# Performance work log

Hardware: AMD Instinct MI355X
Metric: run time of the kernel (lower is better)

Reference implementation:

```python
import jax, jax.numpy as jnp
import numpy as np

B, N, D = 256, 196, 768  # batch, num_patches (14x14 grid), patch_dim (16*16*3)


def setup_inputs() -> dict:
    key = jax.random.key(0)
    k1, k2 = jax.random.split(key)
    features = jax.random.normal(k1, (B, N, D), dtype=jnp.float32)
    position_logits = jax.random.normal(k2, (B, N, N), dtype=jnp.float32)
    return {"features": features, "position_logits": position_logits}


def _rearrange_patches(patches, pos):
    # Deterministic gather form: for each target slot p, take the LARGEST j with
    # pos[i, j] == p, else leave the zero-init.
    b, n, d = patches.shape
    j_ids = jnp.arange(n, dtype=jnp.int32)
    match = pos[:, :, None] == jnp.arange(n)[None, None, :]          # [B, j, p]
    winner = jnp.max(jnp.where(match, j_ids[None, :, None], -1), axis=1)  # [B, p]
    gathered = jnp.take_along_axis(patches, jnp.clip(winner, 0)[:, :, None], axis=1)
    return jnp.where(winner[:, :, None] >= 0, gathered, jnp.zeros((), patches.dtype))


def reference(features, position_logits):
    b, n, d = features.shape
    g = int(n ** 0.5)
    # _get_position_predictions: argmax / max-softmax over dim=1 (position classes)
    pos = jnp.argmax(position_logits, axis=1)                         # [B, N] int
    confidence = jnp.max(jax.nn.softmax(position_logits, axis=1), axis=1)  # [B, N]
    # _rearrange_patches (scatter by predicted position)
    patches = _rearrange_patches(features, pos)
    # _smooth_edges: 3-tap average over interior patch indices, reading originals
    mid = (patches[:, :-2] + patches[:, 1:-1] + patches[:, 2:]) / 3.0
    patches = jnp.concatenate([patches[:, :1], mid, patches[:, -1:]], axis=1)
    # _reconstruct_image: [B, g, g, D] -> [B, D, g, g]
    img = patches.reshape(b, g, g, d).transpose(0, 3, 1, 2)
    return img, confidence
```

## Files before the change

kernel.cpp:

```cpp
#include <hip/hip_runtime.h>
#include <math.h>

#define BB 256
#define NN 196
#define DD 768
#define TDK 32
#define PSTRIDE 204
#define NW 16

typedef float f32x4 __attribute__((ext_vector_type(4)));

__global__ __launch_bounds__(1024) void pos_conf_kernel(
    const float* __restrict__ logits,
    float* __restrict__ conf_out,
    int* __restrict__ winner_out)
{
    const int b = blockIdx.x;
    const int t = threadIdx.x;
    const int w = t >> 6;
    const int l = t & 63;

    __shared__ float sm[NW][NN];
    __shared__ float ss[NW][NN];
    __shared__ int   si[NW][NN];
    __shared__ int   winner_s[NN];

    if (t < NN) winner_s[t] = -1;

    const int i0 = (49 * w) >> 2;
    const int i1 = (49 * (w + 1)) >> 2;

    if (l < 49) {
        const float* base = logits + (size_t)b * NN * NN + 4 * l;
        f32x4 m = {-INFINITY, -INFINITY, -INFINITY, -INFINITY};
        f32x4 s = {0.f, 0.f, 0.f, 0.f};
        int4 idx = make_int4(0, 0, 0, 0);
        #pragma unroll 4
        for (int i = i0; i < i1; ++i) {
            const f32x4 x = *reinterpret_cast<const f32x4*>(base + (size_t)i * NN);
            f32x4 mn;
            mn.x = fmaxf(m.x, x.x); mn.y = fmaxf(m.y, x.y);
            mn.z = fmaxf(m.z, x.z); mn.w = fmaxf(m.w, x.w);
            idx.x = (x.x > m.x) ? i : idx.x;
            idx.y = (x.y > m.y) ? i : idx.y;
            idx.z = (x.z > m.z) ? i : idx.z;
            idx.w = (x.w > m.w) ? i : idx.w;
            s.x = s.x * __expf(m.x - mn.x) + __expf(x.x - mn.x);
            s.y = s.y * __expf(m.y - mn.y) + __expf(x.y - mn.y);
            s.z = s.z * __expf(m.z - mn.z) + __expf(x.z - mn.z);
            s.w = s.w * __expf(m.w - mn.w) + __expf(x.w - mn.w);
            m = mn;
        }
        const int c = 4 * l;
        sm[w][c + 0] = m.x; ss[w][c + 0] = s.x; si[w][c + 0] = idx.x;
        sm[w][c + 1] = m.y; ss[w][c + 1] = s.y; si[w][c + 1] = idx.y;
        sm[w][c + 2] = m.z; ss[w][c + 2] = s.z; si[w][c + 2] = idx.z;
        sm[w][c + 3] = m.w; ss[w][c + 3] = s.w; si[w][c + 3] = idx.w;
    }
    __syncthreads();

    if (t < NN) {
        const int j = t;
        float m = -INFINITY;
        int idx = 0;
        #pragma unroll
        for (int ww = 0; ww < NW; ++ww) {
            const float mg = sm[ww][j];
            if (mg > m) { m = mg; idx = si[ww][j]; }
        }
        float s = 0.0f;
        #pragma unroll
        for (int ww = 0; ww < NW; ++ww)
            s += ss[ww][j] * __expf(sm[ww][j] - m);
        conf_out[b * NN + j] = 1.0f / s;
        atomicMax(&winner_s[idx], j);
    }
    __syncthreads();
    if (t < NN) winner_out[b * NN + t] = winner_s[t];
}

__global__ __launch_bounds__(256) void rearrange_kernel(
    const float* __restrict__ features,
    const int* __restrict__ winner,
    float* __restrict__ img)
{
    const int b  = blockIdx.y;
    const int d0 = blockIdx.x * TDK;
    const int t  = threadIdx.x;

    __shared__ float tile[TDK][PSTRIDE];

    const float* fb = features + (size_t)b * NN * DD;
    const int* wb = winner + b * NN;

    int w[7];
    #pragma unroll
    for (int i = 0; i < 7; ++i) {
        const int r = (t >> 3) + 32 * i;
        w[i] = (r < NN) ? wb[r] : -1;
    }

    const int d4 = (t & 7) * 4;
    #pragma unroll
    for (int i = 0; i < 7; ++i) {
        const int r = (t >> 3) + 32 * i;
        if (r < NN) {
            float4 v = make_float4(0.f, 0.f, 0.f, 0.f);
            if (w[i] >= 0)
                v = *reinterpret_cast<const float4*>(fb + (size_t)w[i] * DD + d0 + d4);
            tile[d4 + 0][r] = v.x;
            tile[d4 + 1][r] = v.y;
            tile[d4 + 2][r] = v.z;
            tile[d4 + 3][r] = v.w;
        }
    }
    __syncthreads();

    #pragma unroll
    for (int it = 0; it < 7; ++it) {
        const int q = t + 256 * it;
        if (q < TDK * 49) {
            const int d = q / 49;
            const int c = q - 49 * d;
            const int p0 = 4 * c;
            const float4 ctr = *reinterpret_cast<const float4*>(&tile[d][p0]);
            const float left  = tile[d][p0 > 0 ? p0 - 1 : 0];
            const float right = tile[d][p0 + 4 < NN ? p0 + 4 : NN - 1];
            f32x4 o;
            o.x = (p0 == 0)          ? ctr.x : (left  + ctr.x + ctr.y) * (1.0f / 3.0f);
            o.y = (ctr.x + ctr.y + ctr.z) * (1.0f / 3.0f);
            o.z = (ctr.y + ctr.z + ctr.w) * (1.0f / 3.0f);
            o.w = (p0 + 3 == NN - 1) ? ctr.w : (ctr.z + ctr.w + right) * (1.0f / 3.0f);
            float* dst = img + (size_t)b * DD * NN + (size_t)(d0 + d) * NN + p0;
            __builtin_nontemporal_store(o, reinterpret_cast<f32x4*>(dst));
        }
    }
}

extern "C" void kernel_launch(void* const* d_in, const int* in_sizes, int n_in,
                              void* d_out, int out_size, void* d_ws, size_t ws_size,
                              hipStream_t stream) {
    const float* features = (const float*)d_in[0];
    const float* logits   = (const float*)d_in[1];

    float* out  = (float*)d_out;
    float* img  = out;
    float* conf = out + (size_t)BB * DD * NN;
    int*   winner = (int*)d_ws;

    pos_conf_kernel<<<BB, 1024, 0, stream>>>(logits, conf, winner);

    dim3 grid(DD / TDK, BB);
    rearrange_kernel<<<grid, 256, 0, stream>>>(features, winner, img);
}
```

Before: 53.65 us.

## Fuse position argmax and rearrange/smooth into one per-batch kernel

After: 50.53 us. 1.06x faster.

```diff
diff --git a/kernel.cpp b/kernel.cpp
--- a/kernel.cpp
+++ b/kernel.cpp
@@ -5,57 +5,62 @@
 #define NN 196
 #define DD 768
 #define TDK 32
+#define NTILES (DD / TDK)
 #define PSTRIDE 204
 #define NW 16
 
 typedef float f32x4 __attribute__((ext_vector_type(4)));
 
-__global__ __launch_bounds__(1024) void pos_conf_kernel(
+__global__ __launch_bounds__(1024) void fused_kernel(
+    const float* __restrict__ features,
     const float* __restrict__ logits,
-    float* __restrict__ conf_out,
-    int* __restrict__ winner_out)
+    float* __restrict__ img,
+    float* __restrict__ conf_out)
 {
     const int b = blockIdx.x;
     const int t = threadIdx.x;
-    const int w = t >> 6;
-    const int l = t & 63;
 
     __shared__ float sm[NW][NN];
     __shared__ float ss[NW][NN];
     __shared__ int   si[NW][NN];
     __shared__ int   winner_s[NN];
+    __shared__ float tile[TDK][PSTRIDE];
+
+    const int wv = t >> 6;
+    const int l  = t & 63;
 
     if (t < NN) winner_s[t] = -1;
 
-    const int i0 = (49 * w) >> 2;
-    const int i1 = (49 * (w + 1)) >> 2;
-
-    if (l < 49) {
-        const float* base = logits + (size_t)b * NN * NN + 4 * l;
-        f32x4 m = {-INFINITY, -INFINITY, -INFINITY, -INFINITY};
-        f32x4 s = {0.f, 0.f, 0.f, 0.f};
-        int4 idx = make_int4(0, 0, 0, 0);
-        #pragma unroll 4
-        for (int i = i0; i < i1; ++i) {
-            const f32x4 x = *reinterpret_cast<const f32x4*>(base + (size_t)i * NN);
-            f32x4 mn;
-            mn.x = fmaxf(m.x, x.x); mn.y = fmaxf(m.y, x.y);
-            mn.z = fmaxf(m.z, x.z); mn.w = fmaxf(m.w, x.w);
-            idx.x = (x.x > m.x) ? i : idx.x;
-            idx.y = (x.y > m.y) ? i : idx.y;
-            idx.z = (x.z > m.z) ? i : idx.z;
-            idx.w = (x.w > m.w) ? i : idx.w;
-            s.x = s.x * __expf(m.x - mn.x) + __expf(x.x - mn.x);
-            s.y = s.y * __expf(m.y - mn.y) + __expf(x.y - mn.y);
-            s.z = s.z * __expf(m.z - mn.z) + __expf(x.z - mn.z);
-            s.w = s.w * __expf(m.w - mn.w) + __expf(x.w - mn.w);
-            m = mn;
+    {
+        const int i0 = (49 * wv) >> 2;
+        const int i1 = (49 * (wv + 1)) >> 2;
+        if (l < 49) {
+            const float* basep = logits + (size_t)b * NN * NN + 4 * l;
+            f32x4 m = {-INFINITY, -INFINITY, -INFINITY, -INFINITY};
+            f32x4 s = {0.f, 0.f, 0.f, 0.f};
+            int4 idx = make_int4(0, 0, 0, 0);
+            #pragma unroll 4
+            for (int i = i0; i < i1; ++i) {
+                const f32x4 x = *reinterpret_cast<const f32x4*>(basep + (size_t)i * NN);
+                f32x4 mn;
+                mn.x = fmaxf(m.x, x.x); mn.y = fmaxf(m.y, x.y);
+                mn.z = fmaxf(m.z, x.z); mn.w = fmaxf(m.w, x.w);
+                idx.x = (x.x > m.x) ? i : idx.x;
+                idx.y = (x.y > m.y) ? i : idx.y;
+                idx.z = (x.z > m.z) ? i : idx.z;
+                idx.w = (x.w > m.w) ? i : idx.w;
+                s.x = s.x * __expf(m.x - mn.x) + __expf(x.x - mn.x);
+                s.y = s.y * __expf(m.y - mn.y) + __expf(x.y - mn.y);
+                s.z = s.z * __expf(m.z - mn.z) + __expf(x.z - mn.z);
+                s.w = s.w * __expf(m.w - mn.w) + __expf(x.w - mn.w);
+                m = mn;
+            }
+            const int c = 4 * l;
+            sm[wv][c + 0] = m.x; ss[wv][c + 0] = s.x; si[wv][c + 0] = idx.x;
+            sm[wv][c + 1] = m.y; ss[wv][c + 1] = s.y; si[wv][c + 1] = idx.y;
+            sm[wv][c + 2] = m.z; ss[wv][c + 2] = s.z; si[wv][c + 2] = idx.z;
+            sm[wv][c + 3] = m.w; ss[wv][c + 3] = s.w; si[wv][c + 3] = idx.w;
         }
-        const int c = 4 * l;
-        sm[w][c + 0] = m.x; ss[w][c + 0] = s.x; si[w][c + 0] = idx.x;
-        sm[w][c + 1] = m.y; ss[w][c + 1] = s.y; si[w][c + 1] = idx.y;
-        sm[w][c + 2] = m.z; ss[w][c + 2] = s.z; si[w][c + 2] = idx.z;
-        sm[w][c + 3] = m.w; ss[w][c + 3] = s.w; si[w][c + 3] = idx.w;
     }
     __syncthreads();
 
@@ -76,64 +81,67 @@
         atomicMax(&winner_s[idx], j);
     }
     __syncthreads();
-    if (t < NN) winner_out[b * NN + t] = winner_s[t];
-}
-
-__global__ __launch_bounds__(256) void rearrange_kernel(
-    const float* __restrict__ features,
-    const int* __restrict__ winner,
-    float* __restrict__ img)
-{
-    const int b  = blockIdx.y;
-    const int d0 = blockIdx.x * TDK;
-    const int t  = threadIdx.x;
-
-    __shared__ float tile[TDK][PSTRIDE];
 
     const float* fb = features + (size_t)b * NN * DD;
-    const int* wb = winner + b * NN;
+    float* ob = img + (size_t)b * DD * NN;
 
-    int w[7];
-    #pragma unroll
-    for (int i = 0; i < 7; ++i) {
-        const int r = (t >> 3) + 32 * i;
-        w[i] = (r < NN) ? wb[r] : -1;
-    }
+    const int q1_ok = (t < 1568 - 1024);
+    const int r0 = t >> 3;
+    const int d40 = (t & 7) * 4;
+    const int r1 = (t + 1024) >> 3;
+    const int d41 = ((t + 1024) & 7) * 4;
 
-    const int d4 = (t & 7) * 4;
-    #pragma unroll
-    for (int i = 0; i < 7; ++i) {
-        const int r = (t >> 3) + 32 * i;
-        if (r < NN) {
-            float4 v = make_float4(0.f, 0.f, 0.f, 0.f);
-            if (w[i] >= 0)
-                v = *reinterpret_cast<const float4*>(fb + (size_t)w[i] * DD + d0 + d4);
-            tile[d4 + 0][r] = v.x;
-            tile[d4 + 1][r] = v.y;
-            tile[d4 + 2][r] = v.z;
-            tile[d4 + 3][r] = v.w;
+    const int w0 = winner_s[r0];
+    const int w1 = q1_ok ? winner_s[r1] : -1;
+
+    const f32x4 zero = {0.f, 0.f, 0.f, 0.f};
+    f32x4 v0 = zero, v1 = zero, nv0 = zero, nv1 = zero;
+
+    if (w0 >= 0) v0 = *reinterpret_cast<const f32x4*>(fb + (size_t)w0 * DD + d40);
+    if (w1 >= 0) v1 = *reinterpret_cast<const f32x4*>(fb + (size_t)w1 * DD + d41);
+
+    for (int k = 0; k < NTILES; ++k) {
+        tile[d40 + 0][r0] = v0.x;
+        tile[d40 + 1][r0] = v0.y;
+        tile[d40 + 2][r0] = v0.z;
+        tile[d40 + 3][r0] = v0.w;
+        if (q1_ok) {
+            tile[d41 + 0][r1] = v1.x;
+            tile[d41 + 1][r1] = v1.y;
+            tile[d41 + 2][r1] = v1.z;
+            tile[d41 + 3][r1] = v1.w;
         }
-    }
-    __syncthreads();
 
-    #pragma unroll
-    for (int it = 0; it < 7; ++it) {
-        const int q = t + 256 * it;
-        if (q < TDK * 49) {
-            const int d = q / 49;
-            const int c = q - 49 * d;
-            const int p0 = 4 * c;
-            const float4 ctr = *reinterpret_cast<const float4*>(&tile[d][p0]);
-            const float left  = tile[d][p0 > 0 ? p0 - 1 : 0];
-            const float right = tile[d][p0 + 4 < NN ? p0 + 4 : NN - 1];
-            f32x4 o;
-            o.x = (p0 == 0)          ? ctr.x : (left  + ctr.x + ctr.y) * (1.0f / 3.0f);
-            o.y = (ctr.x + ctr.y + ctr.z) * (1.0f / 3.0f);
-            o.z = (ctr.y + ctr.z + ctr.w) * (1.0f / 3.0f);
-            o.w = (p0 + 3 == NN - 1) ? ctr.w : (ctr.z + ctr.w + right) * (1.0f / 3.0f);
-            float* dst = img + (size_t)b * DD * NN + (size_t)(d0 + d) * NN + p0;
-            __builtin_nontemporal_store(o, reinterpret_cast<f32x4*>(dst));
+        if (k + 1 < NTILES) {
+            const int d0n = (k + 1) * TDK;
+            nv0 = zero; nv1 = zero;
+            if (w0 >= 0) nv0 = *reinterpret_cast<const f32x4*>(fb + (size_t)w0 * DD + d0n + d40);
+            if (w1 >= 0) nv1 = *reinterpret_cast<const f32x4*>(fb + (size_t)w1 * DD + d0n + d41);
         }
+        __syncthreads();
+
+        const int d0 = k * TDK;
+        #pragma unroll
+        for (int it = 0; it < 2; ++it) {
+            const int q = t + 1024 * it;
+            if (q < TDK * 49) {
+                const int d = q / 49;
+                const int c = q - 49 * d;
+                const int p0 = 4 * c;
+                const f32x4 ctr = *reinterpret_cast<const f32x4*>(&tile[d][p0]);
+                const float left  = tile[d][p0 > 0 ? p0 - 1 : 0];
+                const float right = tile[d][p0 + 4 < NN ? p0 + 4 : NN - 1];
+                f32x4 o;
+                o.x = (p0 == 0)          ? ctr.x : (left  + ctr.x + ctr.y) * (1.0f / 3.0f);
+                o.y = (ctr.x + ctr.y + ctr.z) * (1.0f / 3.0f);
+                o.z = (ctr.y + ctr.z + ctr.w) * (1.0f / 3.0f);
+                o.w = (p0 + 3 == NN - 1) ? ctr.w : (ctr.z + ctr.w + right) * (1.0f / 3.0f);
+                float* dst = ob + (size_t)(d0 + d) * NN + p0;
+                __builtin_nontemporal_store(o, reinterpret_cast<f32x4*>(dst));
+            }
+        }
+        v0 = nv0; v1 = nv1;
+        __syncthreads();
     }
 }
 
@@ -146,10 +154,6 @@
     float* out  = (float*)d_out;
     float* img  = out;
     float* conf = out + (size_t)BB * DD * NN;
-    int*   winner = (int*)d_ws;
 
-    pos_conf_kernel<<<BB, 1024, 0, stream>>>(logits, conf, winner);
-
-    dim3 grid(DD / TDK, BB);
-    rearrange_kernel<<<grid, 256, 0, stream>>>(features, winner, img);
+    fused_kernel<<<BB, 1024, 0, stream>>>(features, logits, img, conf);
 }
```

## Split position kernel across column halves with global atomic winners and swizzled LDS tile

Applied to the files above, without the earlier changes.

Measured after the change: 56.17 us. 1.05x slower.

```diff
diff --git a/kernel.cpp b/kernel.cpp
--- a/kernel.cpp
+++ b/kernel.cpp
@@ -5,134 +5,132 @@
 #define NN 196
 #define DD 768
 #define TDK 32
-#define PSTRIDE 204
-#define NW 16
+#define NTILES (DD / TDK)
+#define SROW 224
+#define NITEMS (NN * 8)
 
 typedef float f32x4 __attribute__((ext_vector_type(4)));
+typedef float f32x2 __attribute__((ext_vector_type(2)));
 
-__global__ __launch_bounds__(1024) void pos_conf_kernel(
+__global__ __launch_bounds__(512) void pos_conf_kernel(
     const float* __restrict__ logits,
     float* __restrict__ conf_out,
-    int* __restrict__ winner_out)
+    int* __restrict__ winner_g)
 {
     const int b = blockIdx.x;
+    const int h = blockIdx.y;
     const int t = threadIdx.x;
-    const int w = t >> 6;
-    const int l = t & 63;
+    const int wv = t >> 6;
+    const int l  = t & 63;
 
-    __shared__ float sm[NW][NN];
-    __shared__ float ss[NW][NN];
-    __shared__ int   si[NW][NN];
-    __shared__ int   winner_s[NN];
+    __shared__ float sm[8][98];
+    __shared__ float ss[8][98];
+    __shared__ int   si[8][98];
 
-    if (t < NN) winner_s[t] = -1;
-
-    const int i0 = (49 * w) >> 2;
-    const int i1 = (49 * (w + 1)) >> 2;
+    const int i0 = (49 * wv) >> 1;
+    const int i1 = (49 * (wv + 1)) >> 1;
 
     if (l < 49) {
-        const float* base = logits + (size_t)b * NN * NN + 4 * l;
-        f32x4 m = {-INFINITY, -INFINITY, -INFINITY, -INFINITY};
-        f32x4 s = {0.f, 0.f, 0.f, 0.f};
-        int4 idx = make_int4(0, 0, 0, 0);
+        const float* basep = logits + (size_t)b * NN * NN + 98 * h + 2 * l;
+        f32x2 m = {-INFINITY, -INFINITY};
+        f32x2 s = {0.f, 0.f};
+        int2 idx = make_int2(0, 0);
         #pragma unroll 4
         for (int i = i0; i < i1; ++i) {
-            const f32x4 x = *reinterpret_cast<const f32x4*>(base + (size_t)i * NN);
-            f32x4 mn;
-            mn.x = fmaxf(m.x, x.x); mn.y = fmaxf(m.y, x.y);
-            mn.z = fmaxf(m.z, x.z); mn.w = fmaxf(m.w, x.w);
+            const f32x2 x = *reinterpret_cast<const f32x2*>(basep + (size_t)i * NN);
+            f32x2 mn;
+            mn.x = fmaxf(m.x, x.x);
+            mn.y = fmaxf(m.y, x.y);
             idx.x = (x.x > m.x) ? i : idx.x;
             idx.y = (x.y > m.y) ? i : idx.y;
-            idx.z = (x.z > m.z) ? i : idx.z;
-            idx.w = (x.w > m.w) ? i : idx.w;
             s.x = s.x * __expf(m.x - mn.x) + __expf(x.x - mn.x);
             s.y = s.y * __expf(m.y - mn.y) + __expf(x.y - mn.y);
-            s.z = s.z * __expf(m.z - mn.z) + __expf(x.z - mn.z);
-            s.w = s.w * __expf(m.w - mn.w) + __expf(x.w - mn.w);
             m = mn;
         }
-        const int c = 4 * l;
-        sm[w][c + 0] = m.x; ss[w][c + 0] = s.x; si[w][c + 0] = idx.x;
-        sm[w][c + 1] = m.y; ss[w][c + 1] = s.y; si[w][c + 1] = idx.y;
-        sm[w][c + 2] = m.z; ss[w][c + 2] = s.z; si[w][c + 2] = idx.z;
-        sm[w][c + 3] = m.w; ss[w][c + 3] = s.w; si[w][c + 3] = idx.w;
+        sm[wv][2 * l + 0] = m.x; ss[wv][2 * l + 0] = s.x; si[wv][2 * l + 0] = idx.x;
+        sm[wv][2 * l + 1] = m.y; ss[wv][2 * l + 1] = s.y; si[wv][2 * l + 1] = idx.y;
     }
     __syncthreads();
 
-    if (t < NN) {
-        const int j = t;
+    if (t < 98) {
         float m = -INFINITY;
         int idx = 0;
         #pragma unroll
-        for (int ww = 0; ww < NW; ++ww) {
-            const float mg = sm[ww][j];
-            if (mg > m) { m = mg; idx = si[ww][j]; }
+        for (int w = 0; w < 8; ++w) {
+            const float mg = sm[w][t];
+            if (mg > m) { m = mg; idx = si[w][t]; }
         }
-        float s = 0.0f;
+        float s = 0.f;
         #pragma unroll
-        for (int ww = 0; ww < NW; ++ww)
-            s += ss[ww][j] * __expf(sm[ww][j] - m);
+        for (int w = 0; w < 8; ++w)
+            s += ss[w][t] * __expf(sm[w][t] - m);
+        const int j = 98 * h + t;
         conf_out[b * NN + j] = 1.0f / s;
-        atomicMax(&winner_s[idx], j);
+        atomicMax(&winner_g[b * NN + idx], j + 1);
     }
-    __syncthreads();
-    if (t < NN) winner_out[b * NN + t] = winner_s[t];
 }
 
 __global__ __launch_bounds__(256) void rearrange_kernel(
     const float* __restrict__ features,
-    const int* __restrict__ winner,
+    const int* __restrict__ winner_g,
     float* __restrict__ img)
 {
+    const int kt = blockIdx.x;
     const int b  = blockIdx.y;
-    const int d0 = blockIdx.x * TDK;
     const int t  = threadIdx.x;
+    const int d0 = kt * TDK;
 
-    __shared__ float tile[TDK][PSTRIDE];
+    __shared__ float tile[TDK * SROW];
 
     const float* fb = features + (size_t)b * NN * DD;
-    const int* wb = winner + b * NN;
+    const int* wb = winner_g + b * NN;
 
-    int w[7];
+    int wn[7], rr[7], k4[7];
     #pragma unroll
     for (int i = 0; i < 7; ++i) {
-        const int r = (t >> 3) + 32 * i;
-        w[i] = (r < NN) ? wb[r] : -1;
+        const int item = t + 256 * i;
+        rr[i] = item >> 3;
+        k4[i] = (item & 7) * 4;
+        wn[i] = (item < NITEMS) ? wb[rr[i]] : 0;
     }
 
-    const int d4 = (t & 7) * 4;
     #pragma unroll
     for (int i = 0; i < 7; ++i) {
-        const int r = (t >> 3) + 32 * i;
-        if (r < NN) {
-            float4 v = make_float4(0.f, 0.f, 0.f, 0.f);
-            if (w[i] >= 0)
-                v = *reinterpret_cast<const float4*>(fb + (size_t)w[i] * DD + d0 + d4);
-            tile[d4 + 0][r] = v.x;
-            tile[d4 + 1][r] = v.y;
-            tile[d4 + 2][r] = v.z;
-            tile[d4 + 3][r] = v.w;
+        const int item = t + 256 * i;
+        if (item < NITEMS) {
+            f32x4 v = {0.f, 0.f, 0.f, 0.f};
+            if (wn[i] > 0)
+                v = *reinterpret_cast<const f32x4*>(fb + (size_t)(wn[i] - 1) * DD + d0 + k4[i]);
+            const int r  = rr[i];
+            const int kb = k4[i] >> 2;
+            const int col = (((r >> 2) ^ kb) << 2) + (r & 3);
+            tile[(k4[i] + 0) * SROW + col] = v.x;
+            tile[(k4[i] + 1) * SROW + col] = v.y;
+            tile[(k4[i] + 2) * SROW + col] = v.z;
+            tile[(k4[i] + 3) * SROW + col] = v.w;
         }
     }
     __syncthreads();
 
+    float* ob = img + (size_t)b * DD * NN + (size_t)d0 * NN;
     #pragma unroll
     for (int it = 0; it < 7; ++it) {
         const int q = t + 256 * it;
-        if (q < TDK * 49) {
-            const int d = q / 49;
-            const int c = q - 49 * d;
+        if (q < NITEMS) {
+            const int dl  = q / 49;
+            const int c   = q - 49 * dl;
+            const int key = (dl >> 2) & 7;
+            const float* row = &tile[dl * SROW];
+            const f32x4 ctr = *reinterpret_cast<const f32x4*>(row + ((c ^ key) << 2));
+            const float left  = (c > 0)  ? row[(((c - 1) ^ key) << 2) + 3] : 0.0f;
+            const float right = (c < 48) ? row[ ((c + 1) ^ key) << 2      ] : 0.0f;
             const int p0 = 4 * c;
-            const float4 ctr = *reinterpret_cast<const float4*>(&tile[d][p0]);
-            const float left  = tile[d][p0 > 0 ? p0 - 1 : 0];
-            const float right = tile[d][p0 + 4 < NN ? p0 + 4 : NN - 1];
             f32x4 o;
             o.x = (p0 == 0)          ? ctr.x : (left  + ctr.x + ctr.y) * (1.0f / 3.0f);
             o.y = (ctr.x + ctr.y + ctr.z) * (1.0f / 3.0f);
             o.z = (ctr.y + ctr.z + ctr.w) * (1.0f / 3.0f);
             o.w = (p0 + 3 == NN - 1) ? ctr.w : (ctr.z + ctr.w + right) * (1.0f / 3.0f);
-            float* dst = img + (size_t)b * DD * NN + (size_t)(d0 + d) * NN + p0;
-            __builtin_nontemporal_store(o, reinterpret_cast<f32x4*>(dst));
+            __builtin_nontemporal_store(o, reinterpret_cast<f32x4*>(ob + (size_t)dl * NN + p0));
         }
     }
 }
@@ -148,8 +146,11 @@
     float* conf = out + (size_t)BB * DD * NN;
     int*   winner = (int*)d_ws;
 
-    pos_conf_kernel<<<BB, 1024, 0, stream>>>(logits, conf, winner);
+    hipMemsetAsync(winner, 0, (size_t)BB * NN * sizeof(int), stream);
 
-    dim3 grid(DD / TDK, BB);
-    rearrange_kernel<<<grid, 256, 0, stream>>>(features, winner, img);
+    dim3 g1(BB, 2);
+    pos_conf_kernel<<<g1, 512, 0, stream>>>(logits, conf, winner);
+
+    dim3 g2(NTILES, BB);
+    rearrange_kernel<<<g2, 256, 0, stream>>>(features, winner, img);
 }
```
